# Optimization experiments

Measured on AMD Instinct MI355X. Metric: run time of the kernel, lower is better.

Reference implementation:

```python
import jax, jax.numpy as jnp
import numpy as np

N_NODES = 20000
N_EDGES = 160000
B = 200      # num graphs (nodes per graph = 100)
T = 8        # num_tau
A = 10       # action_size
H = 4        # heads
D = 128      # out_channels
R = 4        # num_relations
NCOS = 64


def rgat(x, edge_index, edge_type, W, q, k, b):
    # W: [R, in, H*D]; q, k: [H*D, H]; b: [D]
    xw = jnp.einsum('ni,rio->nro', x, W)              # [N, R, H*D]
    src, dst = edge_index[0], edge_index[1]
    xj = xw[src, edge_type]                            # [E, H*D] gather by edge + relation
    xi = xw[dst, edge_type]                            # [E, H*D]
    alpha = jax.nn.leaky_relu(xi @ q + xj @ k, 0.2)    # [E, H]
    amax = jax.ops.segment_max(alpha, dst, num_segments=N_NODES)
    ex = jnp.exp(alpha - amax[dst])                    # segment softmax over dst
    denom = jax.ops.segment_sum(ex, dst, num_segments=N_NODES)
    a = ex / denom[dst]                                # [E, H]
    msg = (a[:, :, None] * xj.reshape(-1, H, D)).reshape(-1, H * D)
    agg = jax.ops.segment_sum(msg, dst, num_segments=N_NODES).reshape(-1, H, D)
    return agg.mean(axis=1) + b                        # concat=False -> mean over heads


def noisy_linear(z, w, bias, sw, sb, ew, eb):
    # torch convention: w [out, in]
    return z @ (w + sw * ew).T + (bias + sb * eb)


def setup_inputs():
    key = jax.random.key(0)
    ks = jax.random.split(key, 48)
    def rn(i, shape, scale=0.05):
        return jax.random.normal(ks[i], shape, dtype=jnp.float32) * scale
    SIG = 0.017
    inp = {
        'x': jax.random.normal(ks[0], (N_NODES, 2), dtype=jnp.float32),
        'edge_index': jax.random.randint(ks[1], (2, N_EDGES), 0, N_NODES, dtype=jnp.int32),
        'edge_type': jax.random.randint(ks[2], (N_EDGES,), 0, R, dtype=jnp.int32),
        'taus': jax.random.uniform(ks[3], (B, T, 1), dtype=jnp.float32),
        'W1': rn(4, (R, 2, H * D), 0.3), 'q1': rn(5, (H * D, H), 0.05), 'k1': rn(6, (H * D, H), 0.05), 'b1': rn(7, (D,)),
        'W2': rn(8, (R, D, H * D), 0.06), 'q2': rn(9, (H * D, H), 0.05), 'k2': rn(10, (H * D, H), 0.05), 'b2': rn(11, (D,)),
        'cos_w': rn(12, (D, NCOS), 0.1), 'cos_b': rn(13, (D,)),
        'ff1_w': rn(14, (D, D), 0.1), 'ff1_b': rn(15, (D,)),
        'ff1_sw': jnp.full((D, D), SIG, jnp.float32), 'ff1_sb': jnp.full((D,), SIG, jnp.float32),
        'ff1_ew': rn(16, (D, D), 1.0), 'ff1_eb': rn(17, (D,), 1.0),
        'ff2_w': rn(18, (D, D), 0.1), 'ff2_b': rn(19, (D,)),
        'ff2_sw': jnp.full((D, D), SIG, jnp.float32), 'ff2_sb': jnp.full((D,), SIG, jnp.float32),
        'ff2_ew': rn(20, (D, D), 1.0), 'ff2_eb': rn(21, (D,), 1.0),
        'adv_w': rn(22, (A, D), 0.1), 'adv_b': rn(23, (A,)),
        'adv_sw': jnp.full((A, D), SIG, jnp.float32), 'adv_sb': jnp.full((A,), SIG, jnp.float32),
        'adv_ew': rn(24, (A, D), 1.0), 'adv_eb': rn(25, (A,), 1.0),
        'val_w': rn(26, (1, D), 0.1), 'val_b': rn(27, (1,)),
        'val_sw': jnp.full((1, D), SIG, jnp.float32), 'val_sb': jnp.full((1,), SIG, jnp.float32),
        'val_ew': rn(28, (1, D), 1.0), 'val_eb': rn(29, (1,), 1.0),
    }
    return inp


def reference(x, edge_index, edge_type, taus,
              W1, q1, k1, b1, W2, q2, k2, b2, cos_w, cos_b,
              ff1_w, ff1_b, ff1_sw, ff1_sb, ff1_ew, ff1_eb,
              ff2_w, ff2_b, ff2_sw, ff2_sb, ff2_ew, ff2_eb,
              adv_w, adv_b, adv_sw, adv_sb, adv_ew, adv_eb,
              val_w, val_b, val_sw, val_sb, val_ew, val_eb):
    h = jax.nn.selu(rgat(x, edge_index, edge_type, W1, q1, k1, b1))
    h = jax.nn.selu(rgat(h, edge_index, edge_type, W2, q2, k2, b2))
    g = h.reshape(B, N_NODES // B, D).sum(axis=1)      # global_add_pool (block batch_idx)
    pis = jnp.pi * jnp.arange(1, NCOS + 1, dtype=jnp.float32)  # [NCOS]
    cos = jnp.cos(taus * pis)                           # [B, T, NCOS]
    cos_x = jax.nn.relu(cos @ cos_w.T + cos_b)          # [B, T, D]
    z = (g[:, None, :] * cos_x).reshape(B * T, D)
    z = jax.nn.selu(noisy_linear(z, ff1_w, ff1_b, ff1_sw, ff1_sb, ff1_ew, ff1_eb))
    z = jax.nn.selu(noisy_linear(z, ff2_w, ff2_b, ff2_sw, ff2_sb, ff2_ew, ff2_eb))
    adv = noisy_linear(z, adv_w, adv_b, adv_sw, adv_sb, adv_ew, adv_eb)   # [B*T, A]
    val = noisy_linear(z, val_w, val_b, val_sw, val_sb, val_ew, val_eb)   # [B*T, 1]
    out = val + adv - adv.mean(axis=1, keepdims=True)
    return out.reshape(B, T, A), taus
```

## Files before the change

### kernel.cpp

```cpp
#include <hip/hip_runtime.h>
#include <hip/hip_bf16.h>

constexpr long NN = 20000;
constexpr long NE = 160000;
constexpr long BB = 200;
constexpr long TT = 8;
constexpr long GN = 100;

constexpr long O_FLAG = 0;
constexpr long O_X    = 16;                 constexpr long N_X   = 40000;
constexpr long O_TAU  = O_X + N_X;          constexpr long N_TAU = 1600;
constexpr long O_W1   = O_TAU + N_TAU;      constexpr long N_W1  = 4096;
constexpr long O_Q1   = O_W1 + N_W1;        constexpr long N_Q   = 2048;
constexpr long O_K1   = O_Q1 + N_Q;
constexpr long O_B1   = O_K1 + N_Q;         constexpr long N_B   = 128;
constexpr long O_W2   = O_B1 + N_B;         constexpr long N_W2  = 262144;
constexpr long O_Q2   = O_W2 + N_W2;
constexpr long O_K2   = O_Q2 + N_Q;
constexpr long O_B2   = O_K2 + N_Q;
constexpr long O_CW   = O_B2 + N_B;         constexpr long N_CW  = 8192;
constexpr long O_CB   = O_CW + N_CW;
constexpr long O_F1W  = O_CB + N_B;         constexpr long N_FW  = 16384;
constexpr long O_F1B  = O_F1W + N_FW;
constexpr long O_F1SW = O_F1B + N_B;
constexpr long O_F1SB = O_F1SW + N_FW;
constexpr long O_F1EW = O_F1SB + N_B;
constexpr long O_F1EB = O_F1EW + N_FW;
constexpr long O_F2W  = O_F1EB + N_B;
constexpr long O_F2B  = O_F2W + N_FW;
constexpr long O_F2SW = O_F2B + N_B;
constexpr long O_F2SB = O_F2SW + N_FW;
constexpr long O_F2EW = O_F2SB + N_B;
constexpr long O_F2EB = O_F2EW + N_FW;
constexpr long O_AW   = O_F2EB + N_B;       constexpr long N_AW  = 1280;
constexpr long O_AB   = O_AW + N_AW;        constexpr long N_AB  = 16;
constexpr long O_ASW  = O_AB + N_AB;
constexpr long O_ASB  = O_ASW + N_AW;
constexpr long O_AEW  = O_ASB + N_AB;
constexpr long O_AEB  = O_AEW + N_AW;
constexpr long O_VW   = O_AEB + N_AB;       constexpr long N_VW  = 128;
constexpr long O_VB   = O_VW + N_VW;        constexpr long N_VB  = 16;
constexpr long O_VSW  = O_VB + N_VB;
constexpr long O_VSB  = O_VSW + N_VW;
constexpr long O_VEW  = O_VSB + N_VB;
constexpr long O_VEB  = O_VEW + N_VW;
constexpr long O_WQ1  = O_VEB + N_VB;
constexpr long O_WK1  = O_WQ1 + 32;
constexpr long O_WQ2  = O_WK1 + 32;
constexpr long O_WK2  = O_WQ2 + 2048;
constexpr long O_CF1W = O_WK2 + 2048;
constexpr long O_CF1B = O_CF1W + N_FW;
constexpr long O_CF2W = O_CF1B + N_B;
constexpr long O_CF2B = O_CF2W + N_FW;
constexpr long O_CAW  = O_CF2B + N_B;
constexpr long O_CAB  = O_CAW + N_AW;
constexpr long O_CVW  = O_CAB + N_AB;
constexpr long O_CVB  = O_CVW + N_VW;
constexpr long O_AL1  = O_CVB + N_VB;
constexpr long O_AL2  = O_AL1 + NE*4;
constexpr long O_H1   = O_AL2 + NE*4;
constexpr long O_H2   = O_H1 + NN*128;
constexpr long O_G    = O_H2 + NN*128;
constexpr long O_Z0   = O_G + BB*128;
constexpr long O_Z1   = O_Z0 + BB*TT*128;
constexpr long O_Z2   = O_Z1 + BB*TT*128;
constexpr long O_AGG1 = O_Z2 + BB*TT*128;
constexpr long O_DEG  = O_AGG1;
constexpr long O_CUR  = O_DEG + NN;
constexpr long O_ROWP = O_CUR + NN;
constexpr long O_PERM = O_ROWP + NN + 8;
constexpr long O_AGG2 = O_AGG1 + NN*128;
constexpr long O_DEN1 = O_AGG2 + NN*128;
constexpr long O_DEN2 = O_DEN1 + NN*4;
constexpr long O_AMAX1= O_DEN2 + NN*4;
constexpr long O_AMAX2= O_AMAX1 + NN*4;
constexpr long O_XW2  = O_AMAX2 + NN*4;
constexpr long O_END_TABLE = O_XW2 + (NN*4*512)/2;
constexpr long MPAD   = 20096;
constexpr long O_H1B  = O_END_TABLE;
constexpr long O_W2BT = O_H1B + (MPAD*128)/2;
constexpr long O_END2 = O_W2BT + (2048L*128)/2;
constexpr long O_AQ   = O_END2;
constexpr long O_AK   = O_AQ + NN*16;
constexpr long O_END3 = O_AK + NN*16;

constexpr int EMAX = 128;

#define DEVFN __device__ __forceinline__

typedef __attribute__((ext_vector_type(8))) short bf16x8;
typedef __attribute__((ext_vector_type(4))) float f32x4;

DEVFN float selu_f(float x){ return 1.0507009873554805f * (x > 0.f ? x : 1.6732632423543772f * expm1f(x)); }
DEVFN float lrelu_f(float x){ return x >= 0.f ? x : 0.2f * x; }
DEVFN float bf2f(unsigned short u){ return __uint_as_float(((unsigned)u) << 16); }

__global__ void k_detect(const unsigned short* taus_u16, int* flag){
    if (threadIdx.x == 0){
        int bf = 1;
        for (int i = 0; i < 128; i++){
            if (taus_u16[i] > 0x3F80u){ bf = 0; break; }
        }
        *flag = bf;
    }
}

struct ConvArgs { const void* src[38]; long off[38]; int n[38]; };

__global__ void k_convert(ConvArgs a, float* ws){
    int arr = blockIdx.y;
    long off = a.off[arr];
    if (off < 0) return;
    const void* s = a.src[arr];
    int n = a.n[arr];
    int bf = ((const int*)ws)[0];
    for (int i = blockIdx.x*blockDim.x + threadIdx.x; i < n; i += gridDim.x*blockDim.x){
        float v;
        if (bf){ unsigned short u = ((const unsigned short*)s)[i]; v = bf2f(u); }
        else   { v = ((const float*)s)[i]; }
        ws[off + i] = v;
    }
}

__global__ void k_hist(const int* ei, float* ws){
    long e = (long)blockIdx.x*blockDim.x + threadIdx.x;
    if (e >= NE) return;
    atomicAdd((int*)(ws + O_DEG) + ei[NE + e], 1);
}

__global__ void k_scan(float* ws){
    const int* deg = (const int*)(ws + O_DEG);
    int* rowp = (int*)(ws + O_ROWP);
    __shared__ int part[256];
    int tid = threadIdx.x;
    int base = tid * 79;
    int n = 0; if (base < NN) n = min(79, (int)NN - base);
    int s = 0;
    for (int i = 0; i < n; i++) s += deg[base + i];
    part[tid] = s;
    __syncthreads();
    if (tid == 0){
        int acc = 0;
        for (int i = 0; i < 256; i++){ int t = part[i]; part[i] = acc; acc += t; }
    }
    __syncthreads();
    int acc = part[tid];
    for (int i = 0; i < n; i++){ rowp[base + i] = acc; acc += deg[base + i]; }
    if (tid == 0) rowp[NN] = (int)NE;
}

__global__ void k_scatter(const int* ei, float* ws){
    long e = (long)blockIdx.x*blockDim.x + threadIdx.x;
    if (e >= NE) return;
    int dst = ei[NE + e];
    int pos = atomicAdd((int*)(ws + O_CUR) + dst, 1);
    ((int*)(ws + O_PERM))[((const int*)(ws + O_ROWP))[dst] + pos] = (int)e;
}

__global__ void k_fold(float* ws){
    int task = blockIdx.y;
    int idx = blockIdx.x*blockDim.x + threadIdx.x;
    if (task < 2){
        if (idx >= 32) return;
        int h = idx & 3, ri = idx >> 2;
        const float* W = ws + O_W1 + (long)ri*512;
        const float* Q = ws + (task == 0 ? O_Q1 : O_K1);
        float s = 0.f;
        for (int o = 0; o < 512; o++) s += W[o] * Q[o*4 + h];
        ws[(task == 0 ? O_WQ1 : O_WK1) + idx] = s;
    } else {
        if (idx >= 2048) return;
        int h = idx & 3, ri = idx >> 2;
        const float* W = ws + O_W2 + (long)ri*512;
        const float* Q = ws + (task == 2 ? O_Q2 : O_K2);
        float s = 0.f;
        for (int o = 0; o < 512; o++) s += W[o] * Q[o*4 + h];
        ws[(task == 2 ? O_WQ2 : O_WK2) + idx] = s;
    }
}

__global__ void k_noisy(float* ws){
    const long tw[8] = {O_F1W,O_F2W,O_AW,O_VW, O_F1B,O_F2B,O_AB,O_VB};
    const long ts[8] = {O_F1SW,O_F2SW,O_ASW,O_VSW, O_F1SB,O_F2SB,O_ASB,O_VSB};
    const long te[8] = {O_F1EW,O_F2EW,O_AEW,O_VEW, O_F1EB,O_F2EB,O_AEB,O_VEB};
    const long td[8] = {O_CF1W,O_CF2W,O_CAW,O_CVW, O_CF1B,O_CF2B,O_CAB,O_CVB};
    const int  tn[8] = {16384,16384,1280,128, 128,128,10,1};
    int t = blockIdx.y;
    for (int i = blockIdx.x*blockDim.x + threadIdx.x; i < tn[t]; i += gridDim.x*blockDim.x)
        ws[td[t] + i] = ws[tw[t] + i] + ws[ts[t] + i]*ws[te[t] + i];
}

__global__ void k_w2b(float* ws){
    int idx = blockIdx.x*blockDim.x + threadIdx.x;
    int n = idx & 2047, k = idx >> 11;
    float v = ws[O_W2 + (long)(n >> 9)*65536 + (long)k*512 + (n & 511)];
    ((__hip_bfloat16*)(ws + O_W2BT))[(long)n*128 + k] = __float2bfloat16(v);
}

__global__ void k_zpad(float* ws){
    int i = blockIdx.x*blockDim.x + threadIdx.x;
    if (i < 6144) ws[O_H1B + (20000L*128)/2 + i] = 0.f;
}

__global__ void k_node1(const int* ei, const int* et, float* ws){
    __shared__ float wqk[64];
    __shared__ float alc[EMAX][4];
    __shared__ float xsc[EMAX][2];
    __shared__ int   rtc[EMAX];
    __shared__ float sacc[4][4][2];
    __shared__ float den[4], amax[4];
    __shared__ float mred[2][4];
    int n = blockIdx.x, tid = threadIdx.x;
    const int* rowp = (const int*)(ws + O_ROWP);
    const int* perm = (const int*)(ws + O_PERM);
    int e0 = rowp[n], deg = rowp[n+1] - e0;
    if (tid < 64) wqk[tid] = ws[O_WQ1 + tid];
    if (tid < 32) ((float*)sacc)[tid] = 0.f;
    if (tid < 4) den[tid] = 0.f;
    float xd0 = ws[O_X + (long)n*2], xd1 = ws[O_X + (long)n*2 + 1];
    __syncthreads();
    float mx[4] = {-3.0e38f,-3.0e38f,-3.0e38f,-3.0e38f};
    for (int j0 = 0; j0 < deg; j0 += 128){
        int j = j0 + tid;
        if (j < deg){
            int e = perm[e0 + j];
            int src = ei[e], rt = et[e];
            float xs0 = ws[O_X + (long)src*2], xs1 = ws[O_X + (long)src*2 + 1];
            const float* Wq = wqk + rt*8;
            const float* Wk = wqk + 32 + rt*8;
            #pragma unroll
            for (int h = 0; h < 4; h++){
                float a = lrelu_f(xd0*Wq[h] + xd1*Wq[4+h] + xs0*Wk[h] + xs1*Wk[4+h]);
                if (j < EMAX) alc[j][h] = a;
                mx[h] = fmaxf(mx[h], a);
            }
            if (j < EMAX){ xsc[j][0] = xs0; xsc[j][1] = xs1; rtc[j] = rt; }
        }
    }
    #pragma unroll
    for (int off = 32; off > 0; off >>= 1)
        #pragma unroll
        for (int h = 0; h < 4; h++) mx[h] = fmaxf(mx[h], __shfl_xor(mx[h], off));
    if ((tid & 63) == 0)
        #pragma unroll
        for (int h = 0; h < 4; h++) mred[tid >> 6][h] = mx[h];
    __syncthreads();
    if (tid < 4) amax[tid] = fmaxf(mred[0][tid], mred[1][tid]);
    __syncthreads();
    for (int j0 = 0; j0 < deg; j0 += 128){
        int j = j0 + tid;
        if (j < deg){
            float al[4], xs0, xs1; int rt;
            if (j < EMAX){
                #pragma unroll
                for (int h = 0; h < 4; h++) al[h] = alc[j][h];
                xs0 = xsc[j][0]; xs1 = xsc[j][1]; rt = rtc[j];
            } else {
                int e = perm[e0 + j];
                int src = ei[e]; rt = et[e];
                xs0 = ws[O_X + (long)src*2]; xs1 = ws[O_X + (long)src*2 + 1];
                const float* Wq = wqk + rt*8;
                const float* Wk = wqk + 32 + rt*8;
                #pragma unroll
                for (int h = 0; h < 4; h++)
                    al[h] = lrelu_f(xd0*Wq[h] + xd1*Wq[4+h] + xs0*Wk[h] + xs1*Wk[4+h]);
            }
            #pragma unroll
            for (int h = 0; h < 4; h++){
                float ex = expf(al[h] - amax[h]);
                atomicAdd(&den[h], ex);
                atomicAdd(&sacc[rt][h][0], ex*xs0);
                atomicAdd(&sacc[rt][h][1], ex*xs1);
            }
        }
    }
    __syncthreads();
    int d = tid;
    float rden[4];
    #pragma unroll
    for (int h = 0; h < 4; h++) rden[h] = den[h] > 0.f ? 0.25f/den[h] : 0.f;
    float v = 0.f;
    #pragma unroll
    for (int r = 0; r < 4; r++)
        #pragma unroll
        for (int h = 0; h < 4; h++){
            float w0 = ws[O_W1 + r*1024 +        h*128 + d];
            float w1 = ws[O_W1 + r*1024 + 512  + h*128 + d];
            v += rden[h]*(w0*sacc[r][h][0] + w1*sacc[r][h][1]);
        }
    float out = selu_f(v + ws[O_B1 + d]);
    ws[O_H1 + (long)n*128 + d] = out;
    ((__hip_bfloat16*)(ws + O_H1B))[(long)n*128 + d] = __float2bfloat16(out);
}

__global__ void k_aqk(float* ws){
    __shared__ float wq[128*16];
    __shared__ float wk[128*16];
    __shared__ float hl[16][129];
    int tid = threadIdx.x;
    long nb = (long)blockIdx.x * 16;
    #pragma unroll
    for (int c = 0; c < 8; c++){
        int idx = tid + c*256;
        int i = idx >> 4, o = idx & 15;
        int r = o >> 2, h = o & 3;
        wq[i*16 + o] = ws[O_WQ2 + r*512 + i*4 + h];
        wk[i*16 + o] = ws[O_WK2 + r*512 + i*4 + h];
        hl[idx >> 7][idx & 127] = ws[O_H1 + nb*128 + idx];
    }
    __syncthreads();
    int j = tid >> 4, o = tid & 15;
    float aq = 0.f, ak = 0.f;
    #pragma unroll 4
    for (int i = 0; i < 128; i++){
        float hv = hl[j][i];
        aq += hv * wq[i*16 + o];
        ak += hv * wk[i*16 + o];
    }
    ws[O_AQ + (nb + j)*16 + o] = aq;
    ws[O_AK + (nb + j)*16 + o] = ak;
}

__global__ void k_xw2_mfma(float* ws){
    __shared__ __align__(16) unsigned short Ash[128*128];
    __shared__ __align__(16) unsigned short Bsh[128*128];
    const unsigned short* h1b  = (const unsigned short*)(ws + O_H1B);
    const unsigned short* w2bt = (const unsigned short*)(ws + O_W2BT);
    long bm = (long)blockIdx.x * 128;
    long bn = (long)blockIdx.y * 128;
    int tid = threadIdx.x;
    char* Ac = (char*)Ash; char* Bc = (char*)Bsh;
    #pragma unroll
    for (int i = 0; i < 8; i++){
        int c = tid + i*256;
        int row = c >> 4, kb = (c & 15) * 16;
        int off = row*256 + (kb ^ ((row & 7) << 4));
        *(bf16x8*)(Ac + off) = *(const bf16x8*)&h1b [(bm + row)*128 + (c & 15)*8];
        *(bf16x8*)(Bc + off) = *(const bf16x8*)&w2bt[(bn + row)*128 + (c & 15)*8];
    }
    __syncthreads();
    int w = tid >> 6, lane = tid & 63;
    int wm = (w >> 1) * 64, wn = (w & 1) * 64;
    int r16 = lane & 15, kq = lane >> 4;
    f32x4 acc[4][4] = {};
    #pragma unroll
    for (int ks = 0; ks < 4; ks++){
        int kbyte = ks*64 + kq*16;
        bf16x8 a[4], b[4];
        #pragma unroll
        for (int m = 0; m < 4; m++){
            int row = wm + m*16 + r16;
            a[m] = *(const bf16x8*)(Ac + row*256 + (kbyte ^ ((row & 7) << 4)));
        }
        #pragma unroll
        for (int n = 0; n < 4; n++){
            int row = wn + n*16 + r16;
            b[n] = *(const bf16x8*)(Bc + row*256 + (kbyte ^ ((row & 7) << 4)));
        }
        #pragma unroll
        for (int m = 0; m < 4; m++)
            #pragma unroll
            for (int n = 0; n < 4; n++)
                acc[m][n] = __builtin_amdgcn_mfma_f32_16x16x32_bf16(a[m], b[n], acc[m][n], 0, 0, 0);
    }
    __hip_bfloat16* xb = (__hip_bfloat16*)(ws + O_XW2);
    #pragma unroll
    for (int m = 0; m < 4; m++){
        long gr0 = bm + wm + m*16 + kq*4;
        #pragma unroll
        for (int j = 0; j < 4; j++){
            long gr = gr0 + j;
            if (gr < NN){
                #pragma unroll
                for (int n = 0; n < 4; n++){
                    long gc = bn + wn + n*16 + r16;
                    xb[gr*2048 + gc] = __float2bfloat16(acc[m][n][j]);
                }
            }
        }
    }
}

__global__ void k_node2(const int* ei, const int* et, float* ws){
    __shared__ float aq[16];
    __shared__ float exc[EMAX][4];
    __shared__ int   esrt[EMAX];
    __shared__ float den[4], amax[4];
    __shared__ float mred[2][4];
    int n = blockIdx.x, tid = threadIdx.x;
    const int* rowp = (const int*)(ws + O_ROWP);
    const int* perm = (const int*)(ws + O_PERM);
    int e0 = rowp[n], deg = rowp[n+1] - e0;
    if (tid < 16) aq[tid] = ws[O_AQ + (long)n*16 + tid];
    if (tid < 4) den[tid] = 0.f;
    __syncthreads();
    float mx[4] = {-3.0e38f,-3.0e38f,-3.0e38f,-3.0e38f};
    for (int j0 = 0; j0 < deg; j0 += 128){
        int j = j0 + tid;
        if (j < deg){
            int e = perm[e0 + j];
            int src = ei[e], rt = et[e];
            float4 k4 = *(const float4*)&ws[O_AK + (long)src*16 + rt*4];
            float al0 = lrelu_f(aq[rt*4+0] + k4.x);
            float al1 = lrelu_f(aq[rt*4+1] + k4.y);
            float al2 = lrelu_f(aq[rt*4+2] + k4.z);
            float al3 = lrelu_f(aq[rt*4+3] + k4.w);
            if (j < EMAX){
                exc[j][0]=al0; exc[j][1]=al1; exc[j][2]=al2; exc[j][3]=al3;
                esrt[j] = src*4 + rt;
            }
            mx[0]=fmaxf(mx[0],al0); mx[1]=fmaxf(mx[1],al1);
            mx[2]=fmaxf(mx[2],al2); mx[3]=fmaxf(mx[3],al3);
        }
    }
    #pragma unroll
    for (int off = 32; off > 0; off >>= 1)
        #pragma unroll
        for (int h = 0; h < 4; h++) mx[h] = fmaxf(mx[h], __shfl_xor(mx[h], off));
    if ((tid & 63) == 0)
        #pragma unroll
        for (int h = 0; h < 4; h++) mred[tid >> 6][h] = mx[h];
    __syncthreads();
    if (tid < 4) amax[tid] = fmaxf(mred[0][tid], mred[1][tid]);
    __syncthreads();
    for (int j0 = 0; j0 < deg; j0 += 128){
        int j = j0 + tid;
        if (j < deg && j < EMAX){
            #pragma unroll
            for (int h = 0; h < 4; h++){
                float ex = expf(exc[j][h] - amax[h]);
                exc[j][h] = ex;
                atomicAdd(&den[h], ex);
            }
        } else if (j < deg){
            int e = perm[e0 + j];
            int src = ei[e], rt = et[e];
            float4 k4 = *(const float4*)&ws[O_AK + (long)src*16 + rt*4];
            float al[4] = {lrelu_f(aq[rt*4+0]+k4.x), lrelu_f(aq[rt*4+1]+k4.y),
                           lrelu_f(aq[rt*4+2]+k4.z), lrelu_f(aq[rt*4+3]+k4.w)};
            #pragma unroll
            for (int h = 0; h < 4; h++) atomicAdd(&den[h], expf(al[h]-amax[h]));
        }
    }
    __syncthreads();
    int d = tid;
    const unsigned short* xw2 = (const unsigned short*)(ws + O_XW2);
    float acc[4] = {0.f,0.f,0.f,0.f};
    for (int j = 0; j < deg; j++){
        float ex[4]; long sr;
        if (j < EMAX){
            ex[0]=exc[j][0]; ex[1]=exc[j][1]; ex[2]=exc[j][2]; ex[3]=exc[j][3];
            sr = esrt[j];
        } else {
            int e = perm[e0 + j];
            int src = ei[e], rt = et[e];
            float4 k4 = *(const float4*)&ws[O_AK + (long)src*16 + rt*4];
            ex[0]=expf(lrelu_f(aq[rt*4+0]+k4.x)-amax[0]);
            ex[1]=expf(lrelu_f(aq[rt*4+1]+k4.y)-amax[1]);
            ex[2]=expf(lrelu_f(aq[rt*4+2]+k4.z)-amax[2]);
            ex[3]=expf(lrelu_f(aq[rt*4+3]+k4.w)-amax[3]);
            sr = (long)src*4 + rt;
        }
        const unsigned short* row = xw2 + sr*512;
        #pragma unroll
        for (int h = 0; h < 4; h++) acc[h] += ex[h]*bf2f(row[h*128 + d]);
    }
    float v = 0.f;
    #pragma unroll
    for (int h = 0; h < 4; h++){
        float rden = den[h] > 0.f ? 0.25f/den[h] : 0.f;
        v += acc[h]*rden;
    }
    ws[O_H2 + (long)n*128 + d] = selu_f(v + ws[O_B2 + d]);
}

__global__ void k_pool(float* ws){
    int b = blockIdx.x, d = threadIdx.x;
    float s = 0.f;
    for (int j = 0; j < GN; j++) s += ws[O_H2 + ((long)b*GN + j)*128 + d];
    ws[O_G + (long)b*128 + d] = s;
}

__global__ void k_cosz(float* ws){
    __shared__ float cs[64];
    int bt = blockIdx.x, t = threadIdx.x;
    if (t < 64){
        float tau = ws[O_TAU + bt];
        cs[t] = cosf(tau * (3.14159265358979323846f * (float)(t + 1)));
    }
    __syncthreads();
    int b = bt >> 3;
    const float* cw = ws + O_CW + (long)t*64;
    float s = ws[O_CB + t];
    for (int c = 0; c < 64; c++) s += cs[c]*cw[c];
    s = fmaxf(s, 0.f);
    ws[O_Z0 + (long)bt*128 + t] = ws[O_G + (long)b*128 + t] * s;
}

__global__ void k_ff(float* ws, long o_src, long o_w, long o_b, long o_dst){
    __shared__ float row[128];
    int bt = blockIdx.x, t = threadIdx.x;
    row[t] = ws[o_src + (long)bt*128 + t];
    __syncthreads();
    const float* W = ws + o_w + (long)t*128;
    float s = ws[o_b + t];
    for (int i = 0; i < 128; i++) s += row[i]*W[i];
    ws[o_dst + (long)bt*128 + t] = selu_f(s);
}

__global__ void k_head(float* ws, void* d_out, const void* taus_raw){
    __shared__ float row[128];
    __shared__ float advs[12];
    int bt = blockIdx.x, t = threadIdx.x;
    row[t] = ws[O_Z2 + (long)bt*128 + t];
    row[64 + t] = ws[O_Z2 + (long)bt*128 + 64 + t];
    __syncthreads();
    if (t < 11){
        const float* W = (t < 10) ? (ws + O_CAW + (long)t*128) : (ws + O_CVW);
        float s = (t < 10) ? ws[O_CAB + t] : ws[O_CVB];
        for (int i = 0; i < 128; i++) s += row[i]*W[i];
        advs[t] = s;
    }
    __syncthreads();
    if (t == 0){
        float m = 0.f;
        #pragma unroll
        for (int a = 0; a < 10; a++) m += advs[a];
        m *= 0.1f;
        float val = advs[10];
        int bf = ((const int*)ws)[0];
        if (bf){
            __hip_bfloat16* out = (__hip_bfloat16*)d_out;
            for (int a = 0; a < 10; a++) out[(long)bt*10 + a] = __float2bfloat16(val + advs[a] - m);
            ((unsigned short*)d_out)[16000 + bt] = ((const unsigned short*)taus_raw)[bt];
        } else {
            float* out = (float*)d_out;
            for (int a = 0; a < 10; a++) out[(long)bt*10 + a] = val + advs[a] - m;
            out[16000 + bt] = ((const float*)taus_raw)[bt];
        }
    }
}

extern "C" void kernel_launch(void* const* d_in, const int* in_sizes, int n_in,
                              void* d_out, int out_size, void* d_ws, size_t ws_size,
                              hipStream_t stream){
    (void)in_sizes; (void)n_in; (void)out_size; (void)ws_size;
    float* ws = (float*)d_ws;
    const int* ei = (const int*)d_in[1];
    const int* et = (const int*)d_in[2];

    hipMemsetAsync(ws + O_DEG, 0, (size_t)(2*NN)*4, stream);

    k_detect<<<1, 64, 0, stream>>>((const unsigned short*)d_in[3], (int*)d_ws);

    k_hist<<<625, 256, 0, stream>>>(ei, ws);
    k_scan<<<1, 256, 0, stream>>>(ws);
    k_scatter<<<625, 256, 0, stream>>>(ei, ws);

    ConvArgs ca;
    static const long conv_o[38] = {
        O_X, -1, -1, O_TAU, O_W1, O_Q1, O_K1, O_B1, O_W2, O_Q2, O_K2, O_B2, O_CW, O_CB,
        O_F1W, O_F1B, O_F1SW, O_F1SB, O_F1EW, O_F1EB,
        O_F2W, O_F2B, O_F2SW, O_F2SB, O_F2EW, O_F2EB,
        O_AW, O_AB, O_ASW, O_ASB, O_AEW, O_AEB,
        O_VW, O_VB, O_VSW, O_VSB, O_VEW, O_VEB };
    static const int conv_n[38] = {
        40000, 0, 0, 1600, 4096, 2048, 2048, 128, 262144, 2048, 2048, 128, 8192, 128,
        16384, 128, 16384, 128, 16384, 128,
        16384, 128, 16384, 128, 16384, 128,
        1280, 10, 1280, 10, 1280, 10,
        128, 1, 128, 1, 128, 1 };
    for (int i = 0; i < 38; i++){ ca.src[i] = d_in[i]; ca.off[i] = conv_o[i]; ca.n[i] = conv_n[i]; }
    k_convert<<<dim3(128, 38), 256, 0, stream>>>(ca, ws);

    k_fold<<<dim3(8, 4), 256, 0, stream>>>(ws);
    k_noisy<<<dim3(64, 8), 256, 0, stream>>>(ws);
    k_w2b<<<1024, 256, 0, stream>>>(ws);
    k_zpad<<<24, 256, 0, stream>>>(ws);

    k_node1<<<20000, 128, 0, stream>>>(ei, et, ws);

    k_xw2_mfma<<<dim3(157, 16), 256, 0, stream>>>(ws);
    k_aqk<<<1250, 256, 0, stream>>>(ws);
    k_node2<<<20000, 128, 0, stream>>>(ei, et, ws);

    k_pool<<<200, 128, 0, stream>>>(ws);
    k_cosz<<<1600, 128, 0, stream>>>(ws);
    k_ff<<<1600, 128, 0, stream>>>(ws, O_Z0, O_CF1W, O_CF1B, O_Z1);
    k_ff<<<1600, 128, 0, stream>>>(ws, O_Z1, O_CF2W, O_CF2B, O_Z2);
    k_head<<<1600, 64, 0, stream>>>(ws, d_out, d_in[3]);
}
```

Before: 262.1 us.

## Fuse prep and tail kernels, interleave XW2 heads for vector gathers

Four small setup kernels (q/k folding, noisy-weight combine, W2 bf16 transpose, zero padding) become one multi-phase k_prep launch. The cos-embedding, two feed-forward layers and dueling head become one k_tail kernel that keeps intermediates in shared memory rather than global scratch. The W2 transpose now interleaves heads by output channel, so k_node2 can fetch all four heads for a channel with one 8-byte load per edge instead of four strided 2-byte loads. The aim is fewer launches and better gather efficiency. The risk is that any unseen reader of XW2 that still assumes the old head-major column order would become inconsistent.

```diff
diff --git a/kernel.cpp b/kernel.cpp
--- a/kernel.cpp
+++ b/kernel.cpp
@@ -90,6 +90,7 @@
 
 typedef __attribute__((ext_vector_type(8))) short bf16x8;
 typedef __attribute__((ext_vector_type(4))) float f32x4;
+typedef __attribute__((ext_vector_type(4))) unsigned short u16x4;
 
 DEVFN float selu_f(float x){ return 1.0507009873554805f * (x > 0.f ? x : 1.6732632423543772f * expm1f(x)); }
 DEVFN float lrelu_f(float x){ return x >= 0.f ? x : 0.2f * x; }
@@ -157,49 +158,52 @@
     ((int*)(ws + O_PERM))[((const int*)(ws + O_ROWP))[dst] + pos] = (int)e;
 }
 
-__global__ void k_fold(float* ws){
-    int task = blockIdx.y;
+__global__ void k_prep(float* ws){
+    int phase = blockIdx.y;
     int idx = blockIdx.x*blockDim.x + threadIdx.x;
-    if (task < 2){
-        if (idx >= 32) return;
-        int h = idx & 3, ri = idx >> 2;
-        const float* W = ws + O_W1 + (long)ri*512;
-        const float* Q = ws + (task == 0 ? O_Q1 : O_K1);
+    if (phase == 0){
+        if (idx >= 4160) return;
+        long wsrc, qsrc, dst; int ri, h;
+        if (idx < 64){
+            int t = idx & 31; h = t & 3; ri = t >> 2;
+            wsrc = O_W1 + (long)ri*512;
+            qsrc = (idx < 32) ? O_Q1 : O_K1;
+            dst  = ((idx < 32) ? O_WQ1 : O_WK1) + t;
+        } else {
+            int t = (idx - 64) & 2047; h = t & 3; ri = t >> 2;
+            wsrc = O_W2 + (long)ri*512;
+            qsrc = (idx < 2112) ? O_Q2 : O_K2;
+            dst  = ((idx < 2112) ? O_WQ2 : O_WK2) + t;
+        }
+        const float* W = ws + wsrc;
+        const float* Q = ws + qsrc;
         float s = 0.f;
         for (int o = 0; o < 512; o++) s += W[o] * Q[o*4 + h];
-        ws[(task == 0 ? O_WQ1 : O_WK1) + idx] = s;
+        ws[dst] = s;
+    } else if (phase == 1){
+        const long tw[8] = {O_F1W,O_F2W,O_AW,O_VW, O_F1B,O_F2B,O_AB,O_VB};
+        const long ts[8] = {O_F1SW,O_F2SW,O_ASW,O_VSW, O_F1SB,O_F2SB,O_ASB,O_VSB};
+        const long te[8] = {O_F1EW,O_F2EW,O_AEW,O_VEW, O_F1EB,O_F2EB,O_AEB,O_VEB};
+        const long td[8] = {O_CF1W,O_CF2W,O_CAW,O_CVW, O_CF1B,O_CF2B,O_CAB,O_CVB};
+        const int  tn[8] = {16384,16384,1280,128, 128,128,10,1};
+        const int  tb[8] = {0,16384,32768,34048, 34176,34304,34432,34442};
+        int total = 34443;
+        for (int i = idx; i < total; i += gridDim.x*blockDim.x){
+            int t = 0;
+            #pragma unroll
+            for (int q = 1; q < 8; q++) if (i >= tb[q]) t = q;
+            int j = i - tb[t];
+            if (j < tn[t]) ws[td[t] + j] = ws[tw[t] + j] + ws[ts[t] + j]*ws[te[t] + j];
+        }
+    } else if (phase == 2){
+        if (idx >= 262144) return;
+        int np = idx & 2047, k = idx >> 11;
+        int r = np >> 9, q = np & 511, d = q >> 2, h = q & 3;
+        float v = ws[O_W2 + (long)r*65536 + (long)k*512 + h*128 + d];
+        ((__hip_bfloat16*)(ws + O_W2BT))[(long)np*128 + k] = __float2bfloat16(v);
     } else {
-        if (idx >= 2048) return;
-        int h = idx & 3, ri = idx >> 2;
-        const float* W = ws + O_W2 + (long)ri*512;
-        const float* Q = ws + (task == 2 ? O_Q2 : O_K2);
-        float s = 0.f;
-        for (int o = 0; o < 512; o++) s += W[o] * Q[o*4 + h];
-        ws[(task == 2 ? O_WQ2 : O_WK2) + idx] = s;
-    }
-}
-
-__global__ void k_noisy(float* ws){
-    const long tw[8] = {O_F1W,O_F2W,O_AW,O_VW, O_F1B,O_F2B,O_AB,O_VB};
-    const long ts[8] = {O_F1SW,O_F2SW,O_ASW,O_VSW, O_F1SB,O_F2SB,O_ASB,O_VSB};
-    const long te[8] = {O_F1EW,O_F2EW,O_AEW,O_VEW, O_F1EB,O_F2EB,O_AEB,O_VEB};
-    const long td[8] = {O_CF1W,O_CF2W,O_CAW,O_CVW, O_CF1B,O_CF2B,O_CAB,O_CVB};
-    const int  tn[8] = {16384,16384,1280,128, 128,128,10,1};
-    int t = blockIdx.y;
-    for (int i = blockIdx.x*blockDim.x + threadIdx.x; i < tn[t]; i += gridDim.x*blockDim.x)
-        ws[td[t] + i] = ws[tw[t] + i] + ws[ts[t] + i]*ws[te[t] + i];
-}
-
-__global__ void k_w2b(float* ws){
-    int idx = blockIdx.x*blockDim.x + threadIdx.x;
-    int n = idx & 2047, k = idx >> 11;
-    float v = ws[O_W2 + (long)(n >> 9)*65536 + (long)k*512 + (n & 511)];
-    ((__hip_bfloat16*)(ws + O_W2BT))[(long)n*128 + k] = __float2bfloat16(v);
-}
-
-__global__ void k_zpad(float* ws){
-    int i = blockIdx.x*blockDim.x + threadIdx.x;
-    if (i < 6144) ws[O_H1B + (20000L*128)/2 + i] = 0.f;
+        if (idx < 6144) ws[O_H1B + (20000L*128)/2 + idx] = 0.f;
+    }
 }
 
 __global__ void k_node1(const int* ei, const int* et, float* ws){
@@ -461,9 +465,11 @@
             ex[3]=expf(lrelu_f(aq[rt*4+3]+k4.w)-amax[3]);
             sr = (long)src*4 + rt;
         }
-        const unsigned short* row = xw2 + sr*512;
-        #pragma unroll
-        for (int h = 0; h < 4; h++) acc[h] += ex[h]*bf2f(row[h*128 + d]);
+        u16x4 v = *(const u16x4*)(xw2 + sr*512 + (d << 2));
+        acc[0] += ex[0]*bf2f(v[0]);
+        acc[1] += ex[1]*bf2f(v[1]);
+        acc[2] += ex[2]*bf2f(v[2]);
+        acc[3] += ex[3]*bf2f(v[3]);
     }
     float v = 0.f;
     #pragma unroll
@@ -481,44 +487,43 @@
     ws[O_G + (long)b*128 + d] = s;
 }
 
-__global__ void k_cosz(float* ws){
+__global__ void k_tail(float* ws, void* d_out, const void* taus_raw){
     __shared__ float cs[64];
+    __shared__ float row0[128], row1[128], row2[128];
+    __shared__ float advs[12];
     int bt = blockIdx.x, t = threadIdx.x;
+    int b = bt >> 3;
     if (t < 64){
         float tau = ws[O_TAU + bt];
         cs[t] = cosf(tau * (3.14159265358979323846f * (float)(t + 1)));
     }
     __syncthreads();
-    int b = bt >> 3;
-    const float* cw = ws + O_CW + (long)t*64;
-    float s = ws[O_CB + t];
-    for (int c = 0; c < 64; c++) s += cs[c]*cw[c];
-    s = fmaxf(s, 0.f);
-    ws[O_Z0 + (long)bt*128 + t] = ws[O_G + (long)b*128 + t] * s;
-}
-
-__global__ void k_ff(float* ws, long o_src, long o_w, long o_b, long o_dst){
-    __shared__ float row[128];
-    int bt = blockIdx.x, t = threadIdx.x;
-    row[t] = ws[o_src + (long)bt*128 + t];
-    __syncthreads();
-    const float* W = ws + o_w + (long)t*128;
-    float s = ws[o_b + t];
-    for (int i = 0; i < 128; i++) s += row[i]*W[i];
-    ws[o_dst + (long)bt*128 + t] = selu_f(s);
-}
-
-__global__ void k_head(float* ws, void* d_out, const void* taus_raw){
-    __shared__ float row[128];
-    __shared__ float advs[12];
-    int bt = blockIdx.x, t = threadIdx.x;
-    row[t] = ws[O_Z2 + (long)bt*128 + t];
-    row[64 + t] = ws[O_Z2 + (long)bt*128 + 64 + t];
+    {
+        const float* cw = ws + O_CW + (long)t*64;
+        float s = ws[O_CB + t];
+        for (int c = 0; c < 64; c++) s += cs[c]*cw[c];
+        s = fmaxf(s, 0.f);
+        row0[t] = ws[O_G + (long)b*128 + t] * s;
+    }
+    __syncthreads();
+    {
+        const float* W = ws + O_CF1W + (long)t*128;
+        float s = ws[O_CF1B + t];
+        for (int i = 0; i < 128; i++) s += row0[i]*W[i];
+        row1[t] = selu_f(s);
+    }
+    __syncthreads();
+    {
+        const float* W = ws + O_CF2W + (long)t*128;
+        float s = ws[O_CF2B + t];
+        for (int i = 0; i < 128; i++) s += row1[i]*W[i];
+        row2[t] = selu_f(s);
+    }
     __syncthreads();
     if (t < 11){
         const float* W = (t < 10) ? (ws + O_CAW + (long)t*128) : (ws + O_CVW);
         float s = (t < 10) ? ws[O_CAB + t] : ws[O_CVB];
-        for (int i = 0; i < 128; i++) s += row[i]*W[i];
+        for (int i = 0; i < 128; i++) s += row2[i]*W[i];
         advs[t] = s;
     }
     __syncthreads();
@@ -573,10 +578,7 @@
     for (int i = 0; i < 38; i++){ ca.src[i] = d_in[i]; ca.off[i] = conv_o[i]; ca.n[i] = conv_n[i]; }
     k_convert<<<dim3(128, 38), 256, 0, stream>>>(ca, ws);
 
-    k_fold<<<dim3(8, 4), 256, 0, stream>>>(ws);
-    k_noisy<<<dim3(64, 8), 256, 0, stream>>>(ws);
-    k_w2b<<<1024, 256, 0, stream>>>(ws);
-    k_zpad<<<24, 256, 0, stream>>>(ws);
+    k_prep<<<dim3(1024, 4), 256, 0, stream>>>(ws);
 
     k_node1<<<20000, 128, 0, stream>>>(ei, et, ws);
 
@@ -585,8 +587,5 @@
     k_node2<<<20000, 128, 0, stream>>>(ei, et, ws);
 
     k_pool<<<200, 128, 0, stream>>>(ws);
-    k_cosz<<<1600, 128, 0, stream>>>(ws);
-    k_ff<<<1600, 128, 0, stream>>>(ws, O_Z0, O_CF1W, O_CF1B, O_Z1);
-    k_ff<<<1600, 128, 0, stream>>>(ws, O_Z1, O_CF2W, O_CF2B, O_Z2);
-    k_head<<<1600, 64, 0, stream>>>(ws, d_out, d_in[3]);
-}
+    k_tail<<<1600, 128, 0, stream>>>(ws, d_out, d_in[3]);
+}
```

Measured after the change: 252.9 us. 1.04x faster.
